# Kernel tuning notes

Hardware: AMD Instinct MI355X
Metric: run time of the kernel (lower is better)

The kernel has to match this reference:

```python
import jax, jax.numpy as jnp
import numpy as np

NUM_NODES = 100000
NUM_EDGES = 6400000


def setup_inputs() -> dict:
    key = jax.random.key(0)
    k1, k2 = jax.random.split(key)
    e = jax.random.normal(k1, (NUM_EDGES,), dtype=jnp.float32)
    edge_index = jax.random.randint(k2, (2, NUM_EDGES), 0, NUM_NODES, dtype=jnp.int64)
    return {"e": e, "edge_index": edge_index, "num_nodes": NUM_NODES}


def reference(e, edge_index, num_nodes):
    # Segment softmax of edge scores e over incoming edges per target node.
    target = edge_index[1]
    # scatter-amax with include_self=True on a -1e9-filled buffer
    e_max = jnp.full((num_nodes,), -1e9, dtype=e.dtype).at[target].max(e)
    exp_e = jnp.exp(e - e_max[target])
    sum_exp = jnp.zeros((num_nodes,), dtype=exp_e.dtype).at[target].add(exp_e)
    alpha = exp_e / (sum_exp[target] + 1e-16)
    return alpha
```

## Files before the change

### kernel.cpp

```cpp
#include <hip/hip_runtime.h>


static constexpr int NN = 100000;

typedef float nf4 __attribute__((ext_vector_type(4)));

template <int P, int PART, int B_PER_P, int NB>
__global__ __launch_bounds__(1024)
void scatter_k(const float4* __restrict__ e4, const int4* __restrict__ t4,
               float* __restrict__ priv, int n4) {
    __shared__ float lsum[PART];

    const int i = blockIdx.x;
    int p, c;
    if constexpr (P == 8) {
        const int x = i & 7;
        const int j = i >> 3;
        p = j & 7;
        c = x * 8 + (j >> 3);
    } else {
        const int k = (i & 7) * 64 + (i >> 3);
        p = k % P;
        c = k / P;
        if (c >= B_PER_P) return;
    }
    const int lo = p * PART;

    for (int k = threadIdx.x; k < PART; k += 1024) lsum[k] = 0.0f;
    __syncthreads();

    const int chunk = (n4 + B_PER_P - 1) / B_PER_P;
    const int beg   = c * chunk;
    const int end   = min(beg + chunk, n4);

    for (int idx = beg + (int)threadIdx.x; idx < end; idx += 1024) {
        float4 e = e4[idx];
        int4   t = t4[idx];
        unsigned jx = (unsigned)(t.x - lo);
        unsigned jy = (unsigned)(t.y - lo);
        unsigned jz = (unsigned)(t.z - lo);
        unsigned jw = (unsigned)(t.w - lo);
        if (jx < (unsigned)PART) atomicAdd(&lsum[jx], __expf(e.x));
        if (jy < (unsigned)PART) atomicAdd(&lsum[jy], __expf(e.y));
        if (jz < (unsigned)PART) atomicAdd(&lsum[jz], __expf(e.z));
        if (jw < (unsigned)PART) atomicAdd(&lsum[jw], __expf(e.w));
    }
    __syncthreads();

    float* dst = priv + (size_t)(c * P + p) * PART;
    for (int k = threadIdx.x; k < PART; k += 1024) dst[k] = lsum[k];
}

template <int P, int PART, int B_PER_P>
__global__ void reduce_k(const float* __restrict__ priv, float* __restrict__ inv) {
    int tid = blockIdx.x * blockDim.x + threadIdx.x;
    if (tid >= NN / 4) return;
    const int n  = tid * 4;
    const int p  = n / PART;
    const int j  = n - p * PART;
    const float4* base = (const float4*)(priv + (size_t)p * PART + j);
    float4 s = make_float4(0.f, 0.f, 0.f, 0.f);
    #pragma unroll 5
    for (int k = 0; k < B_PER_P; ++k) {
        float4 v = base[(size_t)k * (P * PART / 4)];
        s.x += v.x; s.y += v.y; s.z += v.z; s.w += v.w;
    }
    float4 r;
    r.x = 1.0f / (s.x + 1e-16f);
    r.y = 1.0f / (s.y + 1e-16f);
    r.z = 1.0f / (s.z + 1e-16f);
    r.w = 1.0f / (s.w + 1e-16f);
    *(float4*)(inv + (size_t)p * PART + j) = r;
}

__global__ void norm_k(const float4* __restrict__ e4, const int4* __restrict__ t4,
                       const float* __restrict__ inv, float4* __restrict__ out4, int n4) {
    const int half = n4 >> 1;
    int i = blockIdx.x * blockDim.x + threadIdx.x;
    if (i >= half) return;
    int i2 = i + half;
    float4 ea = e4[i];
    int4   ta = t4[i];
    float4 eb = e4[i2];
    int4   tb = t4[i2];
    float sax = inv[ta.x], say = inv[ta.y], saz = inv[ta.z], saw = inv[ta.w];
    float sbx = inv[tb.x], sby = inv[tb.y], sbz = inv[tb.z], sbw = inv[tb.w];
    nf4 ra, rb;
    ra.x = __expf(ea.x) * sax;
    ra.y = __expf(ea.y) * say;
    ra.z = __expf(ea.z) * saz;
    ra.w = __expf(ea.w) * saw;
    rb.x = __expf(eb.x) * sbx;
    rb.y = __expf(eb.y) * sby;
    rb.z = __expf(eb.z) * sbz;
    rb.w = __expf(eb.w) * sbw;
    __builtin_nontemporal_store(ra, (nf4*)&out4[i]);
    __builtin_nontemporal_store(rb, (nf4*)&out4[i2]);
}

extern "C" void kernel_launch(void* const* d_in, const int* in_sizes, int n_in,
                              void* d_out, int out_size, void* d_ws, size_t ws_size,
                              hipStream_t stream) {
    const float* e   = (const float*)d_in[0];
    const int*   idx = (const int*)d_in[1];
    const int E  = in_sizes[0];
    const int n4 = E / 4;

    const int*    tgt = idx + E;
    const float4* e4  = (const float4*)e;
    const int4*   t4  = (const int4*)tgt;

    float*  inv  = (float*)d_ws;
    float*  priv = (float*)d_ws + NN;
    float4* out4 = (float4*)d_out;

    constexpr int    P6_PART = 16672;
    constexpr int    P6_BPP  = 85;
    constexpr int    P6_NB   = 512;
    constexpr size_t need6   = ((size_t)NN + (size_t)510 * P6_PART) * sizeof(float);

    if (ws_size >= need6) {
        scatter_k<6, P6_PART, P6_BPP, P6_NB><<<P6_NB, 1024, 0, stream>>>(e4, t4, priv, n4);
        reduce_k <6, P6_PART, P6_BPP><<<(NN / 4 + 255) / 256, 256, 0, stream>>>(priv, inv);
    } else {
        scatter_k<8, 12500, 64, 512><<<512, 1024, 0, stream>>>(e4, t4, priv, n4);
        reduce_k <8, 12500, 64><<<(NN / 4 + 255) / 256, 256, 0, stream>>>(priv, inv);
    }
    norm_k<<<(n4 / 2 + 255) / 256, 256, 0, stream>>>(e4, t4, inv, out4, n4);
}
```

Before: 175.6 us.

## Split node range: first 10k nodes via global atomics, rest via LDS partitions

Replaces the 6/8-partition LDS histogram with a hybrid scheme. The first 10000 target nodes are accumulated with global atomics by one designated block per edge chunk, and the remaining nodes use 8 LDS partitions of 11264 entries. Smaller partitions mean less LDS per block and a smaller private buffer to reduce, which should raise occupancy and cut reduce traffic. In exchange it adds a memset launch and contended global atomics on a hot 10k range.

```diff
diff --git a/kernel.cpp b/kernel.cpp
--- a/kernel.cpp
+++ b/kernel.cpp
@@ -1,30 +1,27 @@
 #include <hip/hip_runtime.h>
 
 
-static constexpr int NN = 100000;
+static constexpr int NN      = 100000;
+static constexpr int G       = 10000;
+static constexpr int P       = 8;
+static constexpr int PART    = 11264;
+static constexpr int B_PER_P = 64;
+static constexpr int NB      = P * B_PER_P;
 
 typedef float nf4 __attribute__((ext_vector_type(4)));
 
-template <int P, int PART, int B_PER_P, int NB>
 __global__ __launch_bounds__(1024)
 void scatter_k(const float4* __restrict__ e4, const int4* __restrict__ t4,
-               float* __restrict__ priv, int n4) {
+               float* __restrict__ priv, float* __restrict__ gsum, int n4) {
     __shared__ float lsum[PART];
 
     const int i = blockIdx.x;
-    int p, c;
-    if constexpr (P == 8) {
-        const int x = i & 7;
-        const int j = i >> 3;
-        p = j & 7;
-        c = x * 8 + (j >> 3);
-    } else {
-        const int k = (i & 7) * 64 + (i >> 3);
-        p = k % P;
-        c = k / P;
-        if (c >= B_PER_P) return;
-    }
-    const int lo = p * PART;
+    const int x = i & 7;
+    const int j = i >> 3;
+    const int p = j & 7;
+    const int c = x * 8 + (j >> 3);
+    const int lo = G + p * PART;
+    const bool rtr = (p == (c & 7));
 
     for (int k = threadIdx.x; k < PART; k += 1024) lsum[k] = 0.0f;
     __syncthreads();
@@ -44,6 +41,12 @@
         if (jy < (unsigned)PART) atomicAdd(&lsum[jy], __expf(e.y));
         if (jz < (unsigned)PART) atomicAdd(&lsum[jz], __expf(e.z));
         if (jw < (unsigned)PART) atomicAdd(&lsum[jw], __expf(e.w));
+        if (rtr) {
+            if ((unsigned)t.x < (unsigned)G) atomicAdd(&gsum[t.x], __expf(e.x));
+            if ((unsigned)t.y < (unsigned)G) atomicAdd(&gsum[t.y], __expf(e.y));
+            if ((unsigned)t.z < (unsigned)G) atomicAdd(&gsum[t.z], __expf(e.z));
+            if ((unsigned)t.w < (unsigned)G) atomicAdd(&gsum[t.w], __expf(e.w));
+        }
     }
     __syncthreads();
 
@@ -51,26 +54,32 @@
     for (int k = threadIdx.x; k < PART; k += 1024) dst[k] = lsum[k];
 }
 
-template <int P, int PART, int B_PER_P>
-__global__ void reduce_k(const float* __restrict__ priv, float* __restrict__ inv) {
+__global__ void reduce_k(const float* __restrict__ priv, const float* __restrict__ gsum,
+                         float* __restrict__ inv) {
     int tid = blockIdx.x * blockDim.x + threadIdx.x;
     if (tid >= NN / 4) return;
-    const int n  = tid * 4;
-    const int p  = n / PART;
-    const int j  = n - p * PART;
-    const float4* base = (const float4*)(priv + (size_t)p * PART + j);
-    float4 s = make_float4(0.f, 0.f, 0.f, 0.f);
-    #pragma unroll 5
-    for (int k = 0; k < B_PER_P; ++k) {
-        float4 v = base[(size_t)k * (P * PART / 4)];
-        s.x += v.x; s.y += v.y; s.z += v.z; s.w += v.w;
+    const int n = tid * 4;
+    float4 s;
+    if (n < G) {
+        s = *(const float4*)(gsum + n);
+    } else {
+        const int m = n - G;
+        const int p = m / PART;
+        const int j = m - p * PART;
+        const float4* base = (const float4*)(priv + (size_t)p * PART + j);
+        s = make_float4(0.f, 0.f, 0.f, 0.f);
+        #pragma unroll 8
+        for (int k = 0; k < B_PER_P; ++k) {
+            float4 v = base[(size_t)k * (P * PART / 4)];
+            s.x += v.x; s.y += v.y; s.z += v.z; s.w += v.w;
+        }
     }
     float4 r;
     r.x = 1.0f / (s.x + 1e-16f);
     r.y = 1.0f / (s.y + 1e-16f);
     r.z = 1.0f / (s.z + 1e-16f);
     r.w = 1.0f / (s.w + 1e-16f);
-    *(float4*)(inv + (size_t)p * PART + j) = r;
+    *(float4*)(inv + n) = r;
 }
 
 __global__ void norm_k(const float4* __restrict__ e4, const int4* __restrict__ t4,
@@ -111,20 +120,13 @@
     const int4*   t4  = (const int4*)tgt;
 
     float*  inv  = (float*)d_ws;
-    float*  priv = (float*)d_ws + NN;
+    float*  gsum = (float*)d_ws + NN;
+    float*  priv = (float*)d_ws + NN + G;
     float4* out4 = (float4*)d_out;
 
-    constexpr int    P6_PART = 16672;
-    constexpr int    P6_BPP  = 85;
-    constexpr int    P6_NB   = 512;
-    constexpr size_t need6   = ((size_t)NN + (size_t)510 * P6_PART) * sizeof(float);
+    hipMemsetAsync(gsum, 0, (size_t)G * sizeof(float), stream);
 
-    if (ws_size >= need6) {
-        scatter_k<6, P6_PART, P6_BPP, P6_NB><<<P6_NB, 1024, 0, stream>>>(e4, t4, priv, n4);
-        reduce_k <6, P6_PART, P6_BPP><<<(NN / 4 + 255) / 256, 256, 0, stream>>>(priv, inv);
-    } else {
-        scatter_k<8, 12500, 64, 512><<<512, 1024, 0, stream>>>(e4, t4, priv, n4);
-        reduce_k <8, 12500, 64><<<(NN / 4 + 255) / 256, 256, 0, stream>>>(priv, inv);
-    }
-    norm_k<<<(n4 / 2 + 255) / 256, 256, 0, stream>>>(e4, t4, inv, out4, n4);
+    scatter_k<<<NB, 1024, 0, stream>>>(e4, t4, priv, gsum, n4);
+    reduce_k <<<(NN / 4 + 255) / 256, 256, 0, stream>>>(priv, gsum, inv);
+    norm_k   <<<(n4 / 2 + 255) / 256, 256, 0, stream>>>(e4, t4, inv, out4, n4);
 }
```

Result: slower. 201.0 us (+14.5%).
